# Performance work log

Measured on AMD Instinct MI355X. Metric: run time of the kernel, lower is better.

Reference implementation:

```python
import jax, jax.numpy as jnp
import numpy as np

B, N, D, H, L = 2, 1024, 256, 4, 6
DH = D // H          # head dim 64
RDIM = DH // 2       # AxialRotaryEmbedding dim = 32 -> output feature size DH
THETA = 0.01


def setup_inputs() -> dict:
    key = jax.random.key(0)
    ks = iter(jax.random.split(key, 80))
    def nrm(shape, s=1.0):
        return jax.random.normal(next(ks), shape, jnp.float32) * s
    size = jnp.array([1024.0, 768.0], jnp.float32)
    inp = {
        'kpts0': jax.random.uniform(next(ks), (B, N, 2), jnp.float32) * size,
        'kpts1': jax.random.uniform(next(ks), (B, N, 2), jnp.float32) * size,
        'desc0': nrm((B, N, D)),
        'desc1': nrm((B, N, D)),
        'fx': 1.0 / (THETA ** (jnp.arange(0, RDIM, 2, dtype=jnp.float32) / RDIM)),
        'fy': 1.0 / (THETA ** (jnp.arange(0, RDIM, 2, dtype=jnp.float32) / RDIM)),
    }
    s = D ** -0.5
    for p in ('s', 'c'):
        inp[f'{p}_Wqk'] = nrm((L, D, D), s); inp[f'{p}_bqk'] = jnp.zeros((L, D))
        inp[f'{p}_Wv'] = nrm((L, D, D), s);  inp[f'{p}_bv'] = jnp.zeros((L, D))
        inp[f'{p}_Wo'] = nrm((L, D, D), s);  inp[f'{p}_bo'] = jnp.zeros((L, D))
        inp[f'{p}_W1'] = nrm((L, 2 * D, 2 * D), (2 * D) ** -0.5); inp[f'{p}_b1'] = jnp.zeros((L, 2 * D))
        inp[f'{p}_g'] = jnp.ones((L, 2 * D)); inp[f'{p}_be'] = jnp.zeros((L, 2 * D))
        inp[f'{p}_W2'] = nrm((L, 2 * D, D), (2 * D) ** -0.5); inp[f'{p}_b2'] = jnp.zeros((L, D))
    inp['Wp'] = nrm((D, D), s); inp['bp'] = jnp.zeros((D,))
    inp['Wm'] = nrm((D, 1), s); inp['bm'] = jnp.zeros((1,))
    return inp


def reference(kpts0, kpts1, desc0, desc1, fx, fy,
              s_Wqk, s_bqk, s_Wv, s_bv, s_Wo, s_bo, s_W1, s_b1, s_g, s_be, s_W2, s_b2,
              c_Wqk, c_bqk, c_Wv, c_bv, c_Wo, c_bo, c_W1, c_b1, c_g, c_be, c_W2, c_b2,
              Wp, bp, Wm, bm):
    size = jnp.array([1024.0, 768.0], jnp.float32)
    norm_k = lambda k: (k - size / 2) / (size.max() / 2)
    heads = lambda t: t.reshape(t.shape[0], t.shape[1], H, DH)

    def rope(pos):  # pos [B,N,2] -> cos,sin [B,N,1,DH]
        f = jnp.concatenate([jnp.repeat(pos[..., 0:1] * fx, 2, -1),
                             jnp.repeat(pos[..., 1:2] * fy, 2, -1)], -1)[:, :, None, :]
        return jnp.cos(f), jnp.sin(f)

    def rot_half(x):  # pairs (x0,x1) -> (-x1,x0)
        return jnp.stack([-x[..., 1::2], x[..., 0::2]], -1).reshape(x.shape)

    def ln(x, g, b):
        mu = x.mean(-1, keepdims=True)
        v = ((x - mu) ** 2).mean(-1, keepdims=True)
        return (x - mu) / jnp.sqrt(v + 1e-5) * g + b

    def ffn(x, m, W1, b1, g, be, W2, b2):  # x + MLP(LN(concat(x,m)))
        h = jnp.concatenate([x, m], -1) @ W1 + b1
        return x + jax.nn.gelu(ln(h, g, be), approximate=False) @ W2 + b2

    cs0, sn0 = rope(norm_k(kpts0))
    cs1, sn1 = rope(norm_k(kpts1))
    x0, x1 = desc0, desc1
    for i in range(L):
        def self_blk(x, cs, sn):  # rotary self-attention, shared qk projection
            qk = heads(x @ s_Wqk[i] + s_bqk[i])
            qr = qk * cs + rot_half(qk) * sn
            v = heads(x @ s_Wv[i] + s_bv[i])
            a = jax.nn.softmax(jnp.einsum('bnhd,bmhd->bhnm', qr, qr) * DH ** -0.5, -1)
            m = jnp.einsum('bhnm,bmhd->bnhd', a, v).reshape(x.shape) @ s_Wo[i] + s_bo[i]
            return ffn(x, m, s_W1[i], s_b1[i], s_g[i], s_be[i], s_W2[i], s_b2[i])
        x0 = self_blk(x0, cs0, sn0)
        x1 = self_blk(x1, cs1, sn1)
        # bidirectional cross-attention (CrossTransformer math path)
        sc = (DH ** -0.5) ** 0.5
        qk0 = heads(x0 @ c_Wqk[i] + c_bqk[i]) * sc
        qk1 = heads(x1 @ c_Wqk[i] + c_bqk[i]) * sc
        v0 = heads(x0 @ c_Wv[i] + c_bv[i])
        v1 = heads(x1 @ c_Wv[i] + c_bv[i])
        sim = jnp.einsum('bnhd,bmhd->bhnm', qk0, qk1)
        m0 = jnp.einsum('bhnm,bmhd->bnhd', jax.nn.softmax(sim, -1), v1).reshape(x0.shape) @ c_Wo[i] + c_bo[i]
        m1 = jnp.einsum('bhnm,bnhd->bmhd', jax.nn.softmax(sim, 2), v0).reshape(x1.shape) @ c_Wo[i] + c_bo[i]
        x0 = ffn(x0, m0, c_W1[i], c_b1[i], c_g[i], c_be[i], c_W2[i], c_b2[i])
        x1 = ffn(x1, m1, c_W1[i], c_b1[i], c_g[i], c_be[i], c_W2[i], c_b2[i])
    # MatchAssignment: sigmoid log double softmax (temp=None, use_sqrt=False -> r=1)
    md0 = (x0 @ Wp + bp) / D ** 0.25
    md1 = (x1 @ Wp + bp) / D ** 0.25
    sim = jnp.einsum('bmd,bnd->bmn', md0, md1)
    z0 = x0 @ Wm + bm  # [B,N,1]
    z1 = x1 @ Wm + bm
    cert = jax.nn.log_sigmoid(z0) + jnp.swapaxes(jax.nn.log_sigmoid(z1), 1, 2)
    core = jax.nn.log_softmax(sim, -1) + jax.nn.log_softmax(sim, 1) + cert
    scores = jnp.zeros((sim.shape[0], N + 1, N + 1), sim.dtype)
    scores = scores.at[:, :N, :N].set(core)
    scores = scores.at[:, :N, N].set(jax.nn.log_sigmoid(-z0[..., 0]))
    scores = scores.at[:, N, :N].set(jax.nn.log_sigmoid(-z1[..., 0]))
    return scores
```

## Files before the change

### kernel.cpp

```cpp
#include <hip/hip_runtime.h>
#include <hip/hip_bf16.h>
#include <math.h>

#define NB 2
#define NN 1024
#define ND 256
#define NL 6
#define NP (NN + 1)
#define NSP 4

typedef unsigned short u16;
typedef __attribute__((ext_vector_type(8))) short bf16x8;
typedef __attribute__((ext_vector_type(4))) float f32x4;

__device__ __forceinline__ u16 f2b(float f) {
    union { float f; unsigned u; } v; v.f = f;
    unsigned r = v.u + 0x7FFFu + ((v.u >> 16) & 1u);
    return (u16)(r >> 16);
}
__device__ __forceinline__ float b2f(u16 b) {
    union { unsigned u; float f; } v; v.u = ((unsigned)b) << 16;
    return v.f;
}
__device__ __forceinline__ float logsigf(float x) {
    return (x >= 0.f) ? -log1pf(expf(-x)) : (x - log1pf(expf(x)));
}

__global__ void rope_cs_kernel(const float* __restrict__ k0p, const float* __restrict__ k1p,
                               const float* __restrict__ fx, const float* __restrict__ fy,
                               float* __restrict__ cs, float* __restrict__ sn) {
    int idx = blockIdx.x * 256 + threadIdx.x;
    int row = idx >> 6, j = idx & 63;
    const float* kp = (row < 2048) ? k0p + (size_t)row * 2 : k1p + (size_t)(row - 2048) * 2;
    float kx = kp[0], ky = kp[1];
    float f;
    if (j < 32) f = ((kx - 512.f) * (1.f / 512.f)) * fx[j >> 1];
    else        f = ((ky - 384.f) * (1.f / 512.f)) * fy[(j - 32) >> 1];
    cs[idx] = cosf(f);
    sn[idx] = sinf(f);
}

__global__ void copyconv_kernel(const float* __restrict__ d0, const float* __restrict__ d1,
                                float* __restrict__ outf, u16* __restrict__ outb) {
    int i = blockIdx.x * 256 + threadIdx.x;
    float v = (i < 524288) ? d0[i] : d1[i - 524288];
    outf[i] = v; outb[i] = f2b(v);
}

struct WP6 {
    const float* s[6];
    u16* d[6];
    unsigned long long oz[6];
};
__global__ void wconvM_kernel(WP6 w, int perT, int K, int N) {
    __shared__ float t[32][33];
    int z = blockIdx.z;
    int p = z / perT, l = z - p * perT;
    const float* W = w.s[p] + (size_t)l * K * N;
    u16* Wt = w.d[p] + (size_t)l * w.oz[p];
    int k0 = blockIdx.y * 32, n0 = blockIdx.x * 32;
    int tx = threadIdx.x, ty = threadIdx.y;
    for (int i = 0; i < 32; i += 8)
        t[ty + i][tx] = W[(size_t)(k0 + ty + i) * N + n0 + tx];
    __syncthreads();
    for (int i = 0; i < 32; i += 8)
        Wt[(size_t)(n0 + ty + i) * K + k0 + tx] = f2b(t[tx][ty + i]);
}

__global__ void biaspack2_kernel(const float* __restrict__ sbqk, const float* __restrict__ sbv,
                                 const float* __restrict__ cbqk, const float* __restrict__ cbv,
                                 float* __restrict__ out) {
    int idx = blockIdx.x * 256 + threadIdx.x;
    if (idx >= 12 * 512) return;
    int z = idx >> 9, c = idx & 511;
    const float* q = (z < 6) ? sbqk + z * 256 : cbqk + (z - 6) * 256;
    const float* v = (z < 6) ? sbv + z * 256 : cbv + (z - 6) * 256;
    out[idx] = (c < 256) ? q[c] : v[c - 256];
}

__global__ __launch_bounds__(256)
void wfuse_kernel(const float* __restrict__ sWo, const float* __restrict__ sW1,
                  const float* __restrict__ cWo, const float* __restrict__ cW1,
                  u16* __restrict__ wfs, u16* __restrict__ wfc) {
    __shared__ u16 As[64 * 72];
    __shared__ u16 Bs[64 * 72];
    int z = blockIdx.z;
    const float* Wo = (z < 6) ? sWo + (size_t)z * 65536 : cWo + (size_t)(z - 6) * 65536;
    const float* W1 = (z < 6) ? sW1 + (size_t)z * 262144 : cW1 + (size_t)(z - 6) * 262144;
    u16* out = (z < 6) ? wfs + (size_t)z * 262144 : wfc + (size_t)(z - 6) * 262144;
    int n0 = blockIdx.y * 64, a0 = blockIdx.x * 64;
    int tid = threadIdx.x, lane = tid & 63, wave = tid >> 6;
    int wm = (wave >> 1) * 32, wn = (wave & 1) * 32;
    int l15 = lane & 15, l4 = lane >> 4;
    f32x4 acc[2][2] = {};
    for (int j0 = 0; j0 < 256; j0 += 64) {
        {
            int nl = tid & 63, jg = tid >> 6;
#pragma unroll
            for (int q = 0; q < 16; ++q) {
                int j = jg * 16 + q;
                As[nl * 72 + j] = f2b(W1[(size_t)(256 + j0 + j) * 512 + n0 + nl]);
            }
        }
        {
            int jl = tid & 63, ag = tid >> 6;
#pragma unroll
            for (int q = 0; q < 16; ++q) {
                int a = ag * 16 + q;
                Bs[a * 72 + jl] = f2b(Wo[(size_t)(a0 + a) * 256 + j0 + jl]);
            }
        }
        __syncthreads();
#pragma unroll
        for (int ks = 0; ks < 2; ++ks) {
            bf16x8 af0 = *(bf16x8*)&As[(wm + l15) * 72 + ks * 32 + l4 * 8];
            bf16x8 af1 = *(bf16x8*)&As[(wm + 16 + l15) * 72 + ks * 32 + l4 * 8];
            bf16x8 bf0 = *(bf16x8*)&Bs[(wn + l15) * 72 + ks * 32 + l4 * 8];
            bf16x8 bf1 = *(bf16x8*)&Bs[(wn + 16 + l15) * 72 + ks * 32 + l4 * 8];
            acc[0][0] = __builtin_amdgcn_mfma_f32_16x16x32_bf16(af0, bf0, acc[0][0], 0, 0, 0);
            acc[0][1] = __builtin_amdgcn_mfma_f32_16x16x32_bf16(af0, bf1, acc[0][1], 0, 0, 0);
            acc[1][0] = __builtin_amdgcn_mfma_f32_16x16x32_bf16(af1, bf0, acc[1][0], 0, 0, 0);
            acc[1][1] = __builtin_amdgcn_mfma_f32_16x16x32_bf16(af1, bf1, acc[1][1], 0, 0, 0);
        }
        __syncthreads();
    }
#pragma unroll
    for (int mi = 0; mi < 2; ++mi)
#pragma unroll
        for (int ni = 0; ni < 2; ++ni)
#pragma unroll
            for (int j = 0; j < 4; ++j) {
                int r = n0 + wm + mi * 16 + l4 * 4 + j;
                int c = a0 + wn + ni * 16 + l15;
                out[(size_t)r * 512 + 256 + c] = f2b(acc[mi][ni][j]);
            }
}

__global__ void bfuse_kernel(const float* __restrict__ sb1, const float* __restrict__ sbo,
                             const float* __restrict__ sW1, const float* __restrict__ cb1,
                             const float* __restrict__ cbo, const float* __restrict__ cW1,
                             float* __restrict__ bfb) {
    int z = blockIdx.y;
    int n = blockIdx.x * 256 + threadIdx.x;
    const float* b1 = (z < 6) ? sb1 + z * 512 : cb1 + (z - 6) * 512;
    const float* bo = (z < 6) ? sbo + z * 256 : cbo + (z - 6) * 256;
    const float* W1 = (z < 6) ? sW1 + (size_t)z * 262144 : cW1 + (size_t)(z - 6) * 262144;
    float acc = b1[n];
    for (int a = 0; a < 256; ++a) acc += bo[a] * W1[(size_t)(256 + a) * 512 + n];
    bfb[z * 512 + n] = acc;
}

__global__ __launch_bounds__(256)
void gemm_mfma(const u16* __restrict__ A, const u16* __restrict__ A2,
               const u16* __restrict__ Bt, const float* __restrict__ bias,
               const float* __restrict__ res, float* __restrict__ Cf, u16* __restrict__ Cb,
               int M, int N, int K, float scale_lo, float scale_hi,
               const float* __restrict__ csp, const float* __restrict__ snp,
               long zsA, long zsB, long zsC) {
    __shared__ u16 As[2][64 * 72];
    __shared__ u16 Bs[2][64 * 72];
    int zb = blockIdx.z;
    A += (size_t)zb * zsA;
    Bt += (size_t)zb * zsB;
    int tid = threadIdx.x;
    int lane = tid & 63, wave = tid >> 6;
    int row0 = blockIdx.y * 64, col0 = blockIdx.x * 64;
    int wm = (wave >> 1) * 32, wn = (wave & 1) * 32;
    int l15 = lane & 15, l4 = lane >> 4;
    f32x4 acc[2][2] = {};
    int srl = tid >> 3, sc8 = (tid & 7) * 8;

    auto loadA = [&](int k0, int it) -> bf16x8 {
        int rr = row0 + srl + it * 32;
        int kg = k0 + sc8;
        const u16* src;
        if (A2) src = (kg < 256) ? &A[(size_t)rr * 256 + kg] : &A2[(size_t)rr * 256 + kg - 256];
        else    src = &A[(size_t)rr * K + kg];
        return *(const bf16x8*)src;
    };
    auto loadB = [&](int k0, int it) -> bf16x8 {
        return *(const bf16x8*)&Bt[(size_t)(col0 + srl + it * 32) * K + k0 + sc8];
    };

    bf16x8 rA0 = loadA(0, 0), rA1 = loadA(0, 1);
    bf16x8 rB0 = loadB(0, 0), rB1 = loadB(0, 1);
    *(bf16x8*)&As[0][srl * 72 + sc8] = rA0;
    *(bf16x8*)&As[0][(srl + 32) * 72 + sc8] = rA1;
    *(bf16x8*)&Bs[0][srl * 72 + sc8] = rB0;
    *(bf16x8*)&Bs[0][(srl + 32) * 72 + sc8] = rB1;
    __syncthreads();

    int nt = K >> 6;
    for (int t = 0; t < nt; ++t) {
        int buf = t & 1;
        bool more = (t + 1) < nt;
        if (more) {
            rA0 = loadA((t + 1) * 64, 0); rA1 = loadA((t + 1) * 64, 1);
            rB0 = loadB((t + 1) * 64, 0); rB1 = loadB((t + 1) * 64, 1);
        }
#pragma unroll
        for (int ks = 0; ks < 2; ++ks) {
            bf16x8 a0 = *(bf16x8*)&As[buf][(wm + l15) * 72 + ks * 32 + l4 * 8];
            bf16x8 a1 = *(bf16x8*)&As[buf][(wm + 16 + l15) * 72 + ks * 32 + l4 * 8];
            bf16x8 b0 = *(bf16x8*)&Bs[buf][(wn + l15) * 72 + ks * 32 + l4 * 8];
            bf16x8 b1 = *(bf16x8*)&Bs[buf][(wn + 16 + l15) * 72 + ks * 32 + l4 * 8];
            acc[0][0] = __builtin_amdgcn_mfma_f32_16x16x32_bf16(a0, b0, acc[0][0], 0, 0, 0);
            acc[0][1] = __builtin_amdgcn_mfma_f32_16x16x32_bf16(a0, b1, acc[0][1], 0, 0, 0);
            acc[1][0] = __builtin_amdgcn_mfma_f32_16x16x32_bf16(a1, b0, acc[1][0], 0, 0, 0);
            acc[1][1] = __builtin_amdgcn_mfma_f32_16x16x32_bf16(a1, b1, acc[1][1], 0, 0, 0);
        }
        if (more) {
            int nb = buf ^ 1;
            *(bf16x8*)&As[nb][srl * 72 + sc8] = rA0;
            *(bf16x8*)&As[nb][(srl + 32) * 72 + sc8] = rA1;
            *(bf16x8*)&Bs[nb][srl * 72 + sc8] = rB0;
            *(bf16x8*)&Bs[nb][(srl + 32) * 72 + sc8] = rB1;
        }
        __syncthreads();
    }
#pragma unroll
    for (int mi = 0; mi < 2; ++mi)
#pragma unroll
        for (int ni = 0; ni < 2; ++ni)
#pragma unroll
            for (int j = 0; j < 4; ++j) {
                int r = row0 + wm + mi * 16 + l4 * 4 + j;
                int c = col0 + wn + ni * 16 + l15;
                float v = acc[mi][ni][j] + (bias ? bias[c] : 0.f);
                float pn = __shfl_xor(v, 1);
                if (csp && c < 256) {
                    float cc = csp[(size_t)r * 64 + (c & 63)];
                    float ss = snp[(size_t)r * 64 + (c & 63)];
                    v = (c & 1) ? (v * cc + pn * ss) : (v * cc - pn * ss);
                }
                v *= (c < 256) ? scale_lo : scale_hi;
                if (res) v += res[(size_t)r * N + c];
                if (Cf) Cf[(size_t)zb * zsC + (size_t)r * N + c] = v;
                if (Cb) Cb[(size_t)r * N + c] = f2b(v);
            }
}

__global__ __launch_bounds__(256)
void combine4_kernel(const float* __restrict__ Op, const float* __restrict__ mp,
                     const float* __restrict__ lp, u16* __restrict__ Ocomb) {
    int idx = blockIdx.x * 256 + threadIdx.x;
    int ri = idx >> 3, dseg = idx & 7;
    int y = ri >> 10, iq = ri & 1023;
    int t = y >> 3, b = (y >> 2) & 1, h = y & 3;
    int rg = t * 2048 + b * 1024 + iq;
    float m[NSP], l[NSP];
    float mf = -1e30f;
#pragma unroll
    for (int s = 0; s < NSP; ++s) {
        m[s] = mp[s * 16384 + ri];
        l[s] = lp[s * 16384 + ri];
        mf = fmaxf(mf, m[s]);
    }
    float e[NSP], denom = 0.f;
#pragma unroll
    for (int s = 0; s < NSP; ++s) { e[s] = __expf(m[s] - mf); denom += l[s] * e[s]; }
    float inv = 1.f / denom;
    float o[8] = {};
#pragma unroll
    for (int s = 0; s < NSP; ++s) {
        size_t base = ((size_t)(s * 16384 + ri)) * 64 + dseg * 8;
        f32x4 a0 = *(const f32x4*)&Op[base];
        f32x4 a1 = *(const f32x4*)&Op[base + 4];
        float w = e[s] * inv;
#pragma unroll
        for (int q = 0; q < 4; ++q) { o[q] += a0[q] * w; o[4 + q] += a1[q] * w; }
    }
    u16 ob[8];
#pragma unroll
    for (int q = 0; q < 8; ++q) ob[q] = f2b(o[q]);
    *(bf16x8*)&Ocomb[(size_t)rg * 256 + h * 64 + dseg * 8] = *(bf16x8*)ob;
}

__global__ __launch_bounds__(256)
void ln_gelu_wave(const u16* __restrict__ hb, const float* __restrict__ g,
                  const float* __restrict__ be, u16* __restrict__ out) {
    int wave = threadIdx.x >> 6, lane = threadIdx.x & 63;
    int row = blockIdx.x * 4 + wave;
    const u16* p = hb + (size_t)row * 512 + lane * 8;
    bf16x8 v = *(const bf16x8*)p;
    float f[8];
    float sum = 0.f, ss = 0.f;
#pragma unroll
    for (int e = 0; e < 8; ++e) {
        f[e] = b2f(((u16*)&v)[e]);
        sum += f[e]; ss += f[e] * f[e];
    }
#pragma unroll
    for (int d = 1; d < 64; d <<= 1) {
        sum += __shfl_xor(sum, d);
        ss  += __shfl_xor(ss, d);
    }
    float mu = sum * (1.f / 512.f);
    float rstd = rsqrtf(ss * (1.f / 512.f) - mu * mu + 1e-5f);
    f32x4 g0 = *(const f32x4*)&g[lane * 8];
    f32x4 g1 = *(const f32x4*)&g[lane * 8 + 4];
    f32x4 b0 = *(const f32x4*)&be[lane * 8];
    f32x4 b1 = *(const f32x4*)&be[lane * 8 + 4];
    u16 o[8];
#pragma unroll
    for (int e = 0; e < 8; ++e) {
        float gg = (e < 4) ? g0[e] : g1[e - 4];
        float bb = (e < 4) ? b0[e] : b1[e - 4];
        float y = (f[e] - mu) * rstd * gg + bb;
        o[e] = f2b(0.5f * y * (1.f + erff(y * 0.70710678118654752f)));
    }
    *(bf16x8*)(out + (size_t)row * 512 + lane * 8) = *(bf16x8*)o;
}

#define QSTR 72
#define VDSTR 1032
#define VBUFE (4 * VDSTR)

__global__ __launch_bounds__(256)
void flash_kernel(const u16* __restrict__ Qp, const u16* __restrict__ Vp,
                  float* __restrict__ Op, float* __restrict__ mp, float* __restrict__ lp,
                  int kswap) {
    __shared__ u16 Ks[2][64 * QSTR];
    __shared__ u16 Vs[2][VBUFE];
    __shared__ u16 Ps[64 * QSTR];
    int y = blockIdx.z;
    int half = blockIdx.y;
    int t = y >> 3, b = (y >> 2) & 1, h = y & 3;
    int qR = t * 2048 + b * 1024;
    int kt = kswap ? (1 - t) : t;
    int kR = kt * 2048 + b * 1024 + half * (NN / NSP);
    int i0 = blockIdx.x * 64;
    int tid = threadIdx.x, lane = tid & 63, wave = tid >> 6;
    int l15 = lane & 15, l4 = lane >> 4;
    int wm = wave * 16;
    int srl = tid >> 3, sc8 = (tid & 7) * 8;

    const u16* Kbase = Qp + (size_t)kR * 512 + h * 64;
    const u16* Vbase = Vp + (size_t)kR * 512 + h * 64;

#pragma unroll
    for (int it = 0; it < 2; ++it) {
        int rr = srl + it * 32;
        *(bf16x8*)&Ks[0][rr * QSTR + sc8] = *(const bf16x8*)&Kbase[(size_t)rr * 512 + sc8];
        bf16x8 v = *(const bf16x8*)&Vbase[(size_t)rr * 512 + sc8];
        *(bf16x8*)&Vs[0][(sc8 >> 4) * VDSTR + rr * 16 + (sc8 & 15)] = v;
    }
    bf16x8 qf[2];
    {
        const u16* qrow = Qp + (size_t)(qR + i0 + wm + l15) * 512 + h * 64;
        qf[0] = *(const bf16x8*)&qrow[l4 * 8];
        qf[1] = *(const bf16x8*)&qrow[32 + l4 * 8];
    }
    __syncthreads();

    float m[4], l[4];
    f32x4 accO[4] = {};
#pragma unroll
    for (int j = 0; j < 4; ++j) { m[j] = -1e30f; l[j] = 0.f; }

    for (int j0 = 0; j0 < NN / NSP; j0 += 64) {
        int buf = (j0 >> 6) & 1;
        bool more = (j0 + 64) < NN / NSP;
        bf16x8 nK0, nK1, nV0, nV1;
        if (more) {
            nK0 = *(const bf16x8*)&Kbase[(size_t)(j0 + 64 + srl) * 512 + sc8];
            nK1 = *(const bf16x8*)&Kbase[(size_t)(j0 + 96 + srl) * 512 + sc8];
            nV0 = *(const bf16x8*)&Vbase[(size_t)(j0 + 64 + srl) * 512 + sc8];
            nV1 = *(const bf16x8*)&Vbase[(size_t)(j0 + 96 + srl) * 512 + sc8];
        }
        f32x4 accS[4] = {};
#pragma unroll
        for (int ks = 0; ks < 2; ++ks) {
#pragma unroll
            for (int n = 0; n < 4; ++n) {
                bf16x8 bb = *(bf16x8*)&Ks[buf][(n * 16 + l15) * QSTR + ks * 32 + l4 * 8];
                accS[n] = __builtin_amdgcn_mfma_f32_16x16x32_bf16(qf[ks], bb, accS[n], 0, 0, 0);
            }
        }
        float p[4][4];
#pragma unroll
        for (int j = 0; j < 4; ++j) {
            float tm = fmaxf(fmaxf(accS[0][j], accS[1][j]), fmaxf(accS[2][j], accS[3][j]));
#pragma unroll
            for (int d = 1; d < 16; d <<= 1) tm = fmaxf(tm, __shfl_xor(tm, d));
            float mnew = fmaxf(m[j], tm);
            float rr = __expf(m[j] - mnew);
            float ts = 0.f;
#pragma unroll
            for (int n = 0; n < 4; ++n) {
                float pv = __expf(accS[n][j] - mnew);
                p[n][j] = pv; ts += pv;
            }
#pragma unroll
            for (int d = 1; d < 16; d <<= 1) ts += __shfl_xor(ts, d);
            l[j] = l[j] * rr + ts;
            m[j] = mnew;
#pragma unroll
            for (int n = 0; n < 4; ++n) accO[n][j] *= rr;
        }
#pragma unroll
        for (int n = 0; n < 4; ++n) {
            int kv = n * 16 + l15;
            int c = (kv & 32) + (((kv >> 2) & 3) << 3) + (((kv >> 4) & 1) << 2) + (kv & 3);
#pragma unroll
            for (int j = 0; j < 4; ++j)
                Ps[(wm + l4 * 4 + j) * QSTR + c] = f2b(p[n][j]);
        }
#pragma unroll
        for (int ks = 0; ks < 2; ++ks) {
            bf16x8 a = *(bf16x8*)&Ps[(wm + l15) * QSTR + ks * 32 + l4 * 8];
#pragma unroll
            for (int n = 0; n < 4; ++n) {
                unsigned va = (unsigned)(size_t)(&Vs[buf][n * VDSTR]) + ks * 1024 + lane * 8;
                unsigned long long q0, q1;
                asm volatile("ds_read_b64_tr_b16 %0, %2\n\t"
                             "ds_read_b64_tr_b16 %1, %2 offset:512\n\t"
                             "s_waitcnt lgkmcnt(0)"
                             : "=&v"(q0), "=&v"(q1) : "v"(va) : "memory");
                union { unsigned long long q[2]; bf16x8 v; } uu;
                uu.q[0] = q0; uu.q[1] = q1;
                accO[n] = __builtin_amdgcn_mfma_f32_16x16x32_bf16(a, uu.v, accO[n], 0, 0, 0);
            }
        }
        if (more) {
            int nb = buf ^ 1;
            *(bf16x8*)&Ks[nb][srl * QSTR + sc8] = nK0;
            *(bf16x8*)&Ks[nb][(srl + 32) * QSTR + sc8] = nK1;
            *(bf16x8*)&Vs[nb][(sc8 >> 4) * VDSTR + srl * 16 + (sc8 & 15)] = nV0;
            *(bf16x8*)&Vs[nb][(sc8 >> 4) * VDSTR + (srl + 32) * 16 + (sc8 & 15)] = nV1;
        }
        __syncthreads();
    }
    size_t obase = (size_t)(half * 16 + y) * 1024 + i0;
#pragma unroll
    for (int n = 0; n < 4; ++n)
#pragma unroll
        for (int j = 0; j < 4; ++j) {
            int r = wm + l4 * 4 + j;
            Op[(obase + r) * 64 + n * 16 + l15] = accO[n][j];
        }
    if (l15 == 0) {
#pragma unroll
        for (int j = 0; j < 4; ++j) {
            int r = wm + l4 * 4 + j;
            mp[obase + r] = m[j];
            lp[obase + r] = l[j];
        }
    }
}

__global__ void rowstats_kernel(const float* __restrict__ S, float* __restrict__ rm,
                                float* __restrict__ rs, int ncols) {
    __shared__ float sb[256];
    int row = blockIdx.x, tid = threadIdx.x;
    const float* p = S + (size_t)row * ncols;
    float m = -1e30f;
    for (int j = tid; j < ncols; j += 256) m = fmaxf(m, p[j]);
    sb[tid] = m; __syncthreads();
    for (int s = 128; s > 0; s >>= 1) { if (tid < s) sb[tid] = fmaxf(sb[tid], sb[tid + s]); __syncthreads(); }
    m = sb[0]; __syncthreads();
    float s = 0;
    for (int j = tid; j < ncols; j += 256) s += __expf(p[j] - m);
    sb[tid] = s; __syncthreads();
    for (int st = 128; st > 0; st >>= 1) { if (tid < st) sb[tid] += sb[tid + st]; __syncthreads(); }
    if (tid == 0) { rm[row] = m; rs[row] = sb[0]; }
}

#define CSCH 8
__global__ void colstats_part(const float* __restrict__ S, float* __restrict__ pm,
                              float* __restrict__ ps) {
    int mat = blockIdx.z;
    int j = blockIdx.x * 256 + threadIdx.x;
    int r0 = blockIdx.y * (NN / CSCH);
    const float* p = S + (size_t)mat * NN * NN + (size_t)r0 * NN + j;
    float m = -1e30f;
    for (int i = 0; i < NN / CSCH; ++i) m = fmaxf(m, p[(size_t)i * NN]);
    float s = 0;
    for (int i = 0; i < NN / CSCH; ++i) s += __expf(p[(size_t)i * NN] - m);
    int o = (mat * CSCH + blockIdx.y) * NN + j;
    pm[o] = m; ps[o] = s;
}
__global__ void colstats_red(const float* __restrict__ pm, const float* __restrict__ ps,
                             float* __restrict__ cm, float* __restrict__ cs) {
    int idx = blockIdx.x * 256 + threadIdx.x;
    int mat = idx >> 10, j = idx & 1023;
    float m = -1e30f;
#pragma unroll
    for (int k = 0; k < CSCH; ++k) m = fmaxf(m, pm[(mat * CSCH + k) * NN + j]);
    float s = 0;
#pragma unroll
    for (int k = 0; k < CSCH; ++k)
        s += ps[(mat * CSCH + k) * NN + j] * __expf(pm[(mat * CSCH + k) * NN + j] - m);
    cm[idx] = m; cs[idx] = s;
}

__global__ void zproj_kernel(const float* __restrict__ X, const float* __restrict__ Wm,
                             const float* __restrict__ bm, float* __restrict__ z) {
    __shared__ float sb[256];
    int row = blockIdx.x, tid = threadIdx.x;
    float v = X[(size_t)row * 256 + tid] * Wm[tid];
    sb[tid] = v; __syncthreads();
    for (int s = 128; s > 0; s >>= 1) { if (tid < s) sb[tid] += sb[tid + s]; __syncthreads(); }
    if (tid == 0) z[row] = sb[0] + bm[0];
}

__global__ void assemble_kernel(const float* __restrict__ sim2, const float* __restrict__ z0,
                                const float* __restrict__ z1, const float* __restrict__ rm,
                                const float* __restrict__ rs, const float* __restrict__ cm,
                                const float* __restrict__ cs, float* __restrict__ out) {
    int idx = blockIdx.x * 256 + threadIdx.x;
    if (idx >= NB * NP * NP) return;
    int b = idx / (NP * NP);
    int rem = idx - b * NP * NP;
    int i = rem / NP, j = rem - i * NP;
    float v;
    if (i < NN && j < NN) {
        float s = sim2[((size_t)b * NN + i) * NN + j];
        float lr = s - rm[b * NN + i] - logf(rs[b * NN + i]);
        float lc = s - cm[b * NN + j] - logf(cs[b * NN + j]);
        v = lr + lc + logsigf(z0[b * NN + i]) + logsigf(z1[b * NN + j]);
    } else if (i < NN) {
        v = logsigf(-z0[b * NN + i]);
    } else if (j < NN) {
        v = logsigf(-z1[b * NN + j]);
    } else {
        v = 0.f;
    }
    out[idx] = v;
}

extern "C" void kernel_launch(void* const* d_in, const int* in_sizes, int n_in,
                              void* d_out, int out_size, void* d_ws, size_t ws_size,
                              hipStream_t stream) {
    auto in = [&](int i) { return (const float*)d_in[i]; };
    const float* kpts0 = in(0);
    const float* kpts1 = in(1);
    const float* desc0 = in(2);
    const float* desc1 = in(3);
    const float* fx = in(4);
    const float* fy = in(5);
    const float* sWqk = in(6);  const float* sbqk = in(7);
    const float* sWv  = in(8);  const float* sbv  = in(9);
    const float* sWo  = in(10); const float* sbo  = in(11);
    const float* sW1  = in(12); const float* sb1  = in(13);
    const float* sg   = in(14); const float* sbe  = in(15);
    const float* sW2  = in(16); const float* sb2  = in(17);
    const float* cWqk = in(18); const float* cbqk = in(19);
    const float* cWv  = in(20); const float* cbv  = in(21);
    const float* cWo  = in(22); const float* cbo  = in(23);
    const float* cW1  = in(24); const float* cb1  = in(25);
    const float* cg   = in(26); const float* cbe  = in(27);
    const float* cW2  = in(28); const float* cb2  = in(29);
    const float* Wp = in(30); const float* bp = in(31);
    const float* Wm = in(32); const float* bm = in(33);

    const int Mst = 2 * NB * NN;
    const size_t SND = (size_t)Mst * ND;

    char* base = (char*)d_ws;
    size_t off = 0;
    auto allocf = [&](size_t n) { float* p = (float*)(base + off); off += ((n * 4 + 255) & ~(size_t)255); return p; };
    auto allocb = [&](size_t n) { u16* p = (u16*)(base + off);   off += ((n * 2 + 255) & ~(size_t)255); return p; };

    float* x    = allocf(SND);
    float* cst  = allocf((size_t)Mst * 64);
    float* snt  = allocf((size_t)Mst * 64);
    float* simb = allocf((size_t)NB * NN * NN);
    float* Opb  = allocf((size_t)NSP * 16384 * 64);
    float* mpb  = allocf((size_t)NSP * 16384);
    float* lpb  = allocf((size_t)NSP * 16384);
    float* z    = allocf(Mst);
    float* st0  = allocf(2048);
    float* st1  = allocf(2048);
    float* st2  = allocf(2048);
    float* st3  = allocf(2048);
    float* pmb  = allocf((size_t)NB * CSCH * NN);
    float* psb  = allocf((size_t)NB * CSCH * NN);
    float* bqv  = allocf((size_t)12 * 512);
    float* bfb  = allocf((size_t)12 * 512);

    u16* xb    = allocb(SND);
    u16* tQVb  = allocb((size_t)Mst * 512);
    u16* ocb   = allocb(SND);
    u16* attnb = allocb(SND);
    u16* hb    = allocb((size_t)Mst * 512);
    u16* hgb   = allocb((size_t)Mst * 512);
    u16* wsqv = allocb((size_t)NL * 512 * 256);
    u16* wcqv = allocb((size_t)NL * 512 * 256);
    u16* wfs  = allocb((size_t)NL * 512 * 512);
    u16* wfc  = allocb((size_t)NL * 512 * 512);
    u16* wsw2 = allocb((size_t)NL * 512 * 256);
    u16* wcw2 = allocb((size_t)NL * 512 * 256);
    u16* wpb  = allocb((size_t)256 * 256);

    {
        WP6 wa = {};
        wa.s[0] = sWqk; wa.d[0] = wsqv;             wa.oz[0] = 512 * 256;
        wa.s[1] = sWv;  wa.d[1] = wsqv + 256 * 256; wa.oz[1] = 512 * 256;
        wa.s[2] = cWqk; wa.d[2] = wcqv;             wa.oz[2] = 512 * 256;
        wa.s[3] = cWv;  wa.d[3] = wcqv + 256 * 256; wa.oz[3] = 512 * 256;
        wa.s[4] = Wp;   wa.d[4] = wpb;              wa.oz[4] = 256 * 256;
        wconvM_kernel<<<dim3(8, 8, 25), dim3(32, 8), 0, stream>>>(wa, 6, 256, 256);
        WP6 wb = {};
        wb.s[0] = sW1; wb.d[0] = wfs; wb.oz[0] = 512 * 512;
        wb.s[1] = cW1; wb.d[1] = wfc; wb.oz[1] = 512 * 512;
        wconvM_kernel<<<dim3(16, 8, 12), dim3(32, 8), 0, stream>>>(wb, 6, 512, 512);
        WP6 wc = {};
        wc.s[0] = sW2; wc.d[0] = wsw2; wc.oz[0] = 512 * 256;
        wc.s[1] = cW2; wc.d[1] = wcw2; wc.oz[1] = 512 * 256;
        wconvM_kernel<<<dim3(8, 16, 12), dim3(32, 8), 0, stream>>>(wc, 6, 512, 256);
    }
    wfuse_kernel<<<dim3(4, 8, 12), 256, 0, stream>>>(sWo, sW1, cWo, cW1, wfs, wfc);
    bfuse_kernel<<<dim3(2, 12), 256, 0, stream>>>(sb1, sbo, sW1, cb1, cbo, cW1, bfb);
    biaspack2_kernel<<<24, 256, 0, stream>>>(sbqk, sbv, cbqk, cbv, bqv);

    rope_cs_kernel<<<1024, 256, 0, stream>>>(kpts0, kpts1, fx, fy, cst, snt);
    copyconv_kernel<<<4096, 256, 0, stream>>>(desc0, desc1, x, xb);

    auto gemm = [&](const u16* A, const u16* A2, const u16* Bt, const float* bias,
                    const float* res, float* Cf, u16* Cb, int M, int N, int K,
                    float slo, float shi, const float* csp, const float* snp,
                    int nz = 1, long zsA = 0, long zsB = 0, long zsC = 0) {
        gemm_mfma<<<dim3(N / 64, M / 64, nz), 256, 0, stream>>>(
            A, A2, Bt, bias, res, Cf, Cb, M, N, K, slo, shi, csp, snp, zsA, zsB, zsC);
    };

    const float sc = 0.35355339059327379f;

    for (int i = 0; i < NL; ++i) {
        const size_t oQV = (size_t)i * 512 * 256;
        const size_t oWF = (size_t)i * 512 * 512;
        const size_t oW2 = (size_t)i * 512 * 256;

        gemm(xb, nullptr, wsqv + oQV, bqv + i * 512, nullptr, nullptr, tQVb,
             Mst, 512, 256, sc, 1.f, cst, snt);
        flash_kernel<<<dim3(16, NSP, 16), 256, 0, stream>>>(tQVb, tQVb + 256, Opb, mpb, lpb, 0);
        combine4_kernel<<<512, 256, 0, stream>>>(Opb, mpb, lpb, ocb);
        gemm(xb, ocb, wfs + oWF, bfb + i * 512, nullptr, nullptr, hb,
             Mst, 512, 512, 1.f, 1.f, nullptr, nullptr);
        ln_gelu_wave<<<Mst / 4, 256, 0, stream>>>(hb, sg + i * 512, sbe + i * 512, hgb);
        gemm(hgb, nullptr, wsw2 + oW2, sb2 + i * ND, x, x, xb,
             Mst, 256, 512, 1.f, 1.f, nullptr, nullptr);

        gemm(xb, nullptr, wcqv + oQV, bqv + (6 + i) * 512, nullptr, nullptr, tQVb,
             Mst, 512, 256, sc, 1.f, nullptr, nullptr);
        flash_kernel<<<dim3(16, NSP, 16), 256, 0, stream>>>(tQVb, tQVb + 256, Opb, mpb, lpb, 1);
        combine4_kernel<<<512, 256, 0, stream>>>(Opb, mpb, lpb, ocb);
        gemm(xb, ocb, wfc + oWF, bfb + (6 + i) * 512, nullptr, nullptr, hb,
             Mst, 512, 512, 1.f, 1.f, nullptr, nullptr);
        ln_gelu_wave<<<Mst / 4, 256, 0, stream>>>(hb, cg + i * 512, cbe + i * 512, hgb);
        gemm(hgb, nullptr, wcw2 + oW2, cb2 + i * ND, x, x, xb,
             Mst, 256, 512, 1.f, 1.f, nullptr, nullptr);
    }

    gemm(xb, nullptr, wpb, bp, nullptr, nullptr, attnb,
         Mst, 256, 256, 0.25f, 0.25f, nullptr, nullptr);
    zproj_kernel<<<Mst, 256, 0, stream>>>(x, Wm, bm, z);
    gemm(attnb, nullptr, attnb + (size_t)2048 * 256, nullptr, nullptr,
         simb, nullptr, 1024, 1024, 256, 1.f, 1.f, nullptr, nullptr,
         2, (long)1024 * 256, (long)1024 * 256, (long)NN * NN);
    rowstats_kernel<<<NB * NN, 256, 0, stream>>>(simb, st0, st1, NN);
    colstats_part<<<dim3(NN / 256, CSCH, NB), 256, 0, stream>>>(simb, pmb, psb);
    colstats_red<<<(NB * NN) / 256, 256, 0, stream>>>(pmb, psb, st2, st3);
    int total = NB * NP * NP;
    assemble_kernel<<<(total + 255) / 256, 256, 0, stream>>>(simb, z, z + 2048, st0, st1,
                                                             st2, st3, (float*)d_out);
}
```

Before: 1.048 ms.

## Split GEMM into 128-row and 64-row variants, head-major QV layout, halve flash splits

Adds a 128x64-tile GEMM kernel for the wide N=512 projections and the similarity GEMM, and keeps a slimmer 64x64 kernel for the N=256 residual GEMMs. The QK/V projection now writes its output head-major (per-head contiguous 64-wide rows), so flash attention reads K/V with a 64-element stride instead of 512. The flash key dimension is split into 2 chunks instead of 4. The goals are more data reuse per tile, better-coalesced attention loads, and less combine work. In exchange the larger tiles and fewer splits cut the number of blocks, which lowers parallelism on a GPU with many CUs.

```diff
diff --git a/kernel.cpp b/kernel.cpp
--- a/kernel.cpp
+++ b/kernel.cpp
@@ -7,7 +7,8 @@
 #define ND 256
 #define NL 6
 #define NP (NN + 1)
-#define NSP 4
+#define NSP 2
+#define VOFF ((size_t)4 * 4096 * 64)
 
 typedef unsigned short u16;
 typedef __attribute__((ext_vector_type(8))) short bf16x8;
@@ -151,23 +152,23 @@
 }
 
 __global__ __launch_bounds__(256)
-void gemm_mfma(const u16* __restrict__ A, const u16* __restrict__ A2,
-               const u16* __restrict__ Bt, const float* __restrict__ bias,
-               const float* __restrict__ res, float* __restrict__ Cf, u16* __restrict__ Cb,
-               int M, int N, int K, float scale_lo, float scale_hi,
-               const float* __restrict__ csp, const float* __restrict__ snp,
-               long zsA, long zsB, long zsC) {
-    __shared__ u16 As[2][64 * 72];
+void gemm128(const u16* __restrict__ A, const u16* __restrict__ A2,
+             const u16* __restrict__ Bt, const float* __restrict__ bias,
+             float* __restrict__ Cf, u16* __restrict__ Cb,
+             int M, int N, int K, float scale_lo, float scale_hi,
+             const float* __restrict__ csp, const float* __restrict__ snp,
+             long zsA, long zsB, long zsC, int hm) {
+    __shared__ u16 As[2][128 * 72];
     __shared__ u16 Bs[2][64 * 72];
     int zb = blockIdx.z;
     A += (size_t)zb * zsA;
     Bt += (size_t)zb * zsB;
     int tid = threadIdx.x;
     int lane = tid & 63, wave = tid >> 6;
-    int row0 = blockIdx.y * 64, col0 = blockIdx.x * 64;
-    int wm = (wave >> 1) * 32, wn = (wave & 1) * 32;
+    int row0 = blockIdx.y * 128, col0 = blockIdx.x * 64;
+    int wr = wave >> 1, wc = wave & 1;
     int l15 = lane & 15, l4 = lane >> 4;
-    f32x4 acc[2][2] = {};
+    f32x4 acc[4][2] = {};
     int srl = tid >> 3, sc8 = (tid & 7) * 8;
 
     auto loadA = [&](int k0, int it) -> bf16x8 {
@@ -182,6 +183,98 @@
         return *(const bf16x8*)&Bt[(size_t)(col0 + srl + it * 32) * K + k0 + sc8];
     };
 
+    bf16x8 rA0 = loadA(0, 0), rA1 = loadA(0, 1), rA2 = loadA(0, 2), rA3 = loadA(0, 3);
+    bf16x8 rB0 = loadB(0, 0), rB1 = loadB(0, 1);
+    *(bf16x8*)&As[0][srl * 72 + sc8] = rA0;
+    *(bf16x8*)&As[0][(srl + 32) * 72 + sc8] = rA1;
+    *(bf16x8*)&As[0][(srl + 64) * 72 + sc8] = rA2;
+    *(bf16x8*)&As[0][(srl + 96) * 72 + sc8] = rA3;
+    *(bf16x8*)&Bs[0][srl * 72 + sc8] = rB0;
+    *(bf16x8*)&Bs[0][(srl + 32) * 72 + sc8] = rB1;
+    __syncthreads();
+
+    int nt = K >> 6;
+    for (int t = 0; t < nt; ++t) {
+        int buf = t & 1;
+        bool more = (t + 1) < nt;
+        if (more) {
+            rA0 = loadA((t + 1) * 64, 0); rA1 = loadA((t + 1) * 64, 1);
+            rA2 = loadA((t + 1) * 64, 2); rA3 = loadA((t + 1) * 64, 3);
+            rB0 = loadB((t + 1) * 64, 0); rB1 = loadB((t + 1) * 64, 1);
+        }
+#pragma unroll
+        for (int ks = 0; ks < 2; ++ks) {
+            bf16x8 b0 = *(bf16x8*)&Bs[buf][(wc * 32 + l15) * 72 + ks * 32 + l4 * 8];
+            bf16x8 b1 = *(bf16x8*)&Bs[buf][(wc * 32 + 16 + l15) * 72 + ks * 32 + l4 * 8];
+#pragma unroll
+            for (int mi = 0; mi < 4; ++mi) {
+                bf16x8 a = *(bf16x8*)&As[buf][(wr * 64 + mi * 16 + l15) * 72 + ks * 32 + l4 * 8];
+                acc[mi][0] = __builtin_amdgcn_mfma_f32_16x16x32_bf16(a, b0, acc[mi][0], 0, 0, 0);
+                acc[mi][1] = __builtin_amdgcn_mfma_f32_16x16x32_bf16(a, b1, acc[mi][1], 0, 0, 0);
+            }
+        }
+        if (more) {
+            int nb = buf ^ 1;
+            *(bf16x8*)&As[nb][srl * 72 + sc8] = rA0;
+            *(bf16x8*)&As[nb][(srl + 32) * 72 + sc8] = rA1;
+            *(bf16x8*)&As[nb][(srl + 64) * 72 + sc8] = rA2;
+            *(bf16x8*)&As[nb][(srl + 96) * 72 + sc8] = rA3;
+            *(bf16x8*)&Bs[nb][srl * 72 + sc8] = rB0;
+            *(bf16x8*)&Bs[nb][(srl + 32) * 72 + sc8] = rB1;
+        }
+        __syncthreads();
+    }
+#pragma unroll
+    for (int mi = 0; mi < 4; ++mi)
+#pragma unroll
+        for (int ni = 0; ni < 2; ++ni)
+#pragma unroll
+            for (int j = 0; j < 4; ++j) {
+                int r = row0 + wr * 64 + mi * 16 + l4 * 4 + j;
+                int c = col0 + wc * 32 + ni * 16 + l15;
+                float v = acc[mi][ni][j] + (bias ? bias[c] : 0.f);
+                float pn = __shfl_xor(v, 1);
+                if (csp && c < 256) {
+                    float cc = csp[(size_t)r * 64 + (c & 63)];
+                    float ss = snp[(size_t)r * 64 + (c & 63)];
+                    v = (c & 1) ? (v * cc + pn * ss) : (v * cc - pn * ss);
+                }
+                v *= (c < 256) ? scale_lo : scale_hi;
+                if (Cf) Cf[(size_t)zb * zsC + (size_t)r * N + c] = v;
+                if (Cb) {
+                    size_t dst;
+                    if (hm) {
+                        int c2 = c & 255;
+                        size_t base = (c < 256) ? 0 : VOFF;
+                        dst = base + ((size_t)(c2 >> 6) * 4096 + r) * 64 + (c2 & 63);
+                    } else dst = (size_t)r * N + c;
+                    Cb[dst] = f2b(v);
+                }
+            }
+}
+
+__global__ __launch_bounds__(256)
+void gemm64(const u16* __restrict__ A, const u16* __restrict__ Bt,
+            const float* __restrict__ bias, const float* __restrict__ res,
+            float* __restrict__ Cf, u16* __restrict__ Cb,
+            int M, int N, int K, float scale) {
+    __shared__ u16 As[2][64 * 72];
+    __shared__ u16 Bs[2][64 * 72];
+    int tid = threadIdx.x;
+    int lane = tid & 63, wave = tid >> 6;
+    int row0 = blockIdx.y * 64, col0 = blockIdx.x * 64;
+    int wm = (wave >> 1) * 32, wn = (wave & 1) * 32;
+    int l15 = lane & 15, l4 = lane >> 4;
+    f32x4 acc[2][2] = {};
+    int srl = tid >> 3, sc8 = (tid & 7) * 8;
+
+    auto loadA = [&](int k0, int it) -> bf16x8 {
+        return *(const bf16x8*)&A[(size_t)(row0 + srl + it * 32) * K + k0 + sc8];
+    };
+    auto loadB = [&](int k0, int it) -> bf16x8 {
+        return *(const bf16x8*)&Bt[(size_t)(col0 + srl + it * 32) * K + k0 + sc8];
+    };
+
     bf16x8 rA0 = loadA(0, 0), rA1 = loadA(0, 1);
     bf16x8 rB0 = loadB(0, 0), rB1 = loadB(0, 1);
     *(bf16x8*)&As[0][srl * 72 + sc8] = rA0;
@@ -226,22 +319,15 @@
             for (int j = 0; j < 4; ++j) {
                 int r = row0 + wm + mi * 16 + l4 * 4 + j;
                 int c = col0 + wn + ni * 16 + l15;
-                float v = acc[mi][ni][j] + (bias ? bias[c] : 0.f);
-                float pn = __shfl_xor(v, 1);
-                if (csp && c < 256) {
-                    float cc = csp[(size_t)r * 64 + (c & 63)];
-                    float ss = snp[(size_t)r * 64 + (c & 63)];
-                    v = (c & 1) ? (v * cc + pn * ss) : (v * cc - pn * ss);
-                }
-                v *= (c < 256) ? scale_lo : scale_hi;
+                float v = (acc[mi][ni][j] + (bias ? bias[c] : 0.f)) * scale;
                 if (res) v += res[(size_t)r * N + c];
-                if (Cf) Cf[(size_t)zb * zsC + (size_t)r * N + c] = v;
+                if (Cf) Cf[(size_t)r * N + c] = v;
                 if (Cb) Cb[(size_t)r * N + c] = f2b(v);
             }
 }
 
 __global__ __launch_bounds__(256)
-void combine4_kernel(const float* __restrict__ Op, const float* __restrict__ mp,
+void combineN_kernel(const float* __restrict__ Op, const float* __restrict__ mp,
                      const float* __restrict__ lp, u16* __restrict__ Ocomb) {
     int idx = blockIdx.x * 256 + threadIdx.x;
     int ri = idx >> 3, dseg = idx & 7;
@@ -317,7 +403,7 @@
 #define VBUFE (4 * VDSTR)
 
 __global__ __launch_bounds__(256)
-void flash_kernel(const u16* __restrict__ Qp, const u16* __restrict__ Vp,
+void flash_kernel(const u16* __restrict__ QV,
                   float* __restrict__ Op, float* __restrict__ mp, float* __restrict__ lp,
                   int kswap) {
     __shared__ u16 Ks[2][64 * QSTR];
@@ -335,19 +421,20 @@
     int wm = wave * 16;
     int srl = tid >> 3, sc8 = (tid & 7) * 8;
 
-    const u16* Kbase = Qp + (size_t)kR * 512 + h * 64;
-    const u16* Vbase = Vp + (size_t)kR * 512 + h * 64;
+    const u16* Qh = QV + (size_t)h * 4096 * 64;
+    const u16* Kbase = Qh + (size_t)kR * 64;
+    const u16* Vbase = QV + VOFF + (size_t)h * 4096 * 64 + (size_t)kR * 64;
 
 #pragma unroll
     for (int it = 0; it < 2; ++it) {
         int rr = srl + it * 32;
-        *(bf16x8*)&Ks[0][rr * QSTR + sc8] = *(const bf16x8*)&Kbase[(size_t)rr * 512 + sc8];
-        bf16x8 v = *(const bf16x8*)&Vbase[(size_t)rr * 512 + sc8];
+        *(bf16x8*)&Ks[0][rr * QSTR + sc8] = *(const bf16x8*)&Kbase[(size_t)rr * 64 + sc8];
+        bf16x8 v = *(const bf16x8*)&Vbase[(size_t)rr * 64 + sc8];
         *(bf16x8*)&Vs[0][(sc8 >> 4) * VDSTR + rr * 16 + (sc8 & 15)] = v;
     }
     bf16x8 qf[2];
     {
-        const u16* qrow = Qp + (size_t)(qR + i0 + wm + l15) * 512 + h * 64;
+        const u16* qrow = Qh + (size_t)(qR + i0 + wm + l15) * 64;
         qf[0] = *(const bf16x8*)&qrow[l4 * 8];
         qf[1] = *(const bf16x8*)&qrow[32 + l4 * 8];
     }
@@ -363,10 +450,10 @@
         bool more = (j0 + 64) < NN / NSP;
         bf16x8 nK0, nK1, nV0, nV1;
         if (more) {
-            nK0 = *(const bf16x8*)&Kbase[(size_t)(j0 + 64 + srl) * 512 + sc8];
-            nK1 = *(const bf16x8*)&Kbase[(size_t)(j0 + 96 + srl) * 512 + sc8];
-            nV0 = *(const bf16x8*)&Vbase[(size_t)(j0 + 64 + srl) * 512 + sc8];
-            nV1 = *(const bf16x8*)&Vbase[(size_t)(j0 + 96 + srl) * 512 + sc8];
+            nK0 = *(const bf16x8*)&Kbase[(size_t)(j0 + 64 + srl) * 64 + sc8];
+            nK1 = *(const bf16x8*)&Kbase[(size_t)(j0 + 96 + srl) * 64 + sc8];
+            nV0 = *(const bf16x8*)&Vbase[(size_t)(j0 + 64 + srl) * 64 + sc8];
+            nV1 = *(const bf16x8*)&Vbase[(size_t)(j0 + 96 + srl) * 64 + sc8];
         }
         f32x4 accS[4] = {};
 #pragma unroll
@@ -580,7 +667,7 @@
     float* bfb  = allocf((size_t)12 * 512);
 
     u16* xb    = allocb(SND);
-    u16* tQVb  = allocb((size_t)Mst * 512);
+    u16* tQVb  = allocb((size_t)8 * 4096 * 64);
     u16* ocb   = allocb(SND);
     u16* attnb = allocb(SND);
     u16* hb    = allocb((size_t)Mst * 512);
@@ -617,12 +704,16 @@
     rope_cs_kernel<<<1024, 256, 0, stream>>>(kpts0, kpts1, fx, fy, cst, snt);
     copyconv_kernel<<<4096, 256, 0, stream>>>(desc0, desc1, x, xb);
 
-    auto gemm = [&](const u16* A, const u16* A2, const u16* Bt, const float* bias,
-                    const float* res, float* Cf, u16* Cb, int M, int N, int K,
-                    float slo, float shi, const float* csp, const float* snp,
+    auto g128 = [&](const u16* A, const u16* A2, const u16* Bt, const float* bias,
+                    float* Cf, u16* Cb, int M, int N, int K, float slo, float shi,
+                    const float* csp, const float* snp, int hm,
                     int nz = 1, long zsA = 0, long zsB = 0, long zsC = 0) {
-        gemm_mfma<<<dim3(N / 64, M / 64, nz), 256, 0, stream>>>(
-            A, A2, Bt, bias, res, Cf, Cb, M, N, K, slo, shi, csp, snp, zsA, zsB, zsC);
+        gemm128<<<dim3(N / 64, M / 128, nz), 256, 0, stream>>>(
+            A, A2, Bt, bias, Cf, Cb, M, N, K, slo, shi, csp, snp, zsA, zsB, zsC, hm);
+    };
+    auto g64 = [&](const u16* A, const u16* Bt, const float* bias, const float* res,
+                   float* Cf, u16* Cb, int M, int N, int K, float scale) {
+        gemm64<<<dim3(N / 64, M / 64), 256, 0, stream>>>(A, Bt, bias, res, Cf, Cb, M, N, K, scale);
     };
 
     const float sc = 0.35355339059327379f;
@@ -632,32 +723,29 @@
         const size_t oWF = (size_t)i * 512 * 512;
         const size_t oW2 = (size_t)i * 512 * 256;
 
-        gemm(xb, nullptr, wsqv + oQV, bqv + i * 512, nullptr, nullptr, tQVb,
-             Mst, 512, 256, sc, 1.f, cst, snt);
-        flash_kernel<<<dim3(16, NSP, 16), 256, 0, stream>>>(tQVb, tQVb + 256, Opb, mpb, lpb, 0);
-        combine4_kernel<<<512, 256, 0, stream>>>(Opb, mpb, lpb, ocb);
-        gemm(xb, ocb, wfs + oWF, bfb + i * 512, nullptr, nullptr, hb,
-             Mst, 512, 512, 1.f, 1.f, nullptr, nullptr);
+        g128(xb, nullptr, wsqv + oQV, bqv + i * 512, nullptr, tQVb,
+             Mst, 512, 256, sc, 1.f, cst, snt, 1);
+        flash_kernel<<<dim3(16, NSP, 16), 256, 0, stream>>>(tQVb, Opb, mpb, lpb, 0);
+        combineN_kernel<<<512, 256, 0, stream>>>(Opb, mpb, lpb, ocb);
+        g128(xb, ocb, wfs + oWF, bfb + i * 512, nullptr, hb,
+             Mst, 512, 512, 1.f, 1.f, nullptr, nullptr, 0);
         ln_gelu_wave<<<Mst / 4, 256, 0, stream>>>(hb, sg + i * 512, sbe + i * 512, hgb);
-        gemm(hgb, nullptr, wsw2 + oW2, sb2 + i * ND, x, x, xb,
-             Mst, 256, 512, 1.f, 1.f, nullptr, nullptr);
-
-        gemm(xb, nullptr, wcqv + oQV, bqv + (6 + i) * 512, nullptr, nullptr, tQVb,
-             Mst, 512, 256, sc, 1.f, nullptr, nullptr);
-        flash_kernel<<<dim3(16, NSP, 16), 256, 0, stream>>>(tQVb, tQVb + 256, Opb, mpb, lpb, 1);
-        combine4_kernel<<<512, 256, 0, stream>>>(Opb, mpb, lpb, ocb);
-        gemm(xb, ocb, wfc + oWF, bfb + (6 + i) * 512, nullptr, nullptr, hb,
-             Mst, 512, 512, 1.f, 1.f, nullptr, nullptr);
+        g64(hgb, wsw2 + oW2, sb2 + i * ND, x, x, xb, Mst, 256, 512, 1.f);
+
+        g128(xb, nullptr, wcqv + oQV, bqv + (6 + i) * 512, nullptr, tQVb,
+             Mst, 512, 256, sc, 1.f, nullptr, nullptr, 1);
+        flash_kernel<<<dim3(16, NSP, 16), 256, 0, stream>>>(tQVb, Opb, mpb, lpb, 1);
+        combineN_kernel<<<512, 256, 0, stream>>>(Opb, mpb, lpb, ocb);
+        g128(xb, ocb, wfc + oWF, bfb + (6 + i) * 512, nullptr, hb,
+             Mst, 512, 512, 1.f, 1.f, nullptr, nullptr, 0);
         ln_gelu_wave<<<Mst / 4, 256, 0, stream>>>(hb, cg + i * 512, cbe + i * 512, hgb);
-        gemm(hgb, nullptr, wcw2 + oW2, cb2 + i * ND, x, x, xb,
-             Mst, 256, 512, 1.f, 1.f, nullptr, nullptr);
-    }
-
-    gemm(xb, nullptr, wpb, bp, nullptr, nullptr, attnb,
-         Mst, 256, 256, 0.25f, 0.25f, nullptr, nullptr);
+        g64(hgb, wcw2 + oW2, cb2 + i * ND, x, x, xb, Mst, 256, 512, 1.f);
+    }
+
+    g64(xb, wpb, bp, nullptr, nullptr, attnb, Mst, 256, 256, 0.25f);
     zproj_kernel<<<Mst, 256, 0, stream>>>(x, Wm, bm, z);
-    gemm(attnb, nullptr, attnb + (size_t)2048 * 256, nullptr, nullptr,
-         simb, nullptr, 1024, 1024, 256, 1.f, 1.f, nullptr, nullptr,
+    g128(attnb, nullptr, attnb + (size_t)2048 * 256, nullptr, simb, nullptr,
+         1024, 1024, 256, 1.f, 1.f, nullptr, nullptr, 0,
          2, (long)1024 * 256, (long)1024 * 256, (long)NN * NN);
     rowstats_kernel<<<NB * NN, 256, 0, stream>>>(simb, st0, st1, NN);
     colstats_part<<<dim3(NN / 256, CSCH, NB), 256, 0, stream>>>(simb, pmb, psb);
```

After: 1.119 ms. 6.7% more time.
